# Performance work log

Hardware: AMD Instinct MI355X
Metric: run time of the kernel (lower is better)

The kernel has to match this reference:

```python
import math
import jax, jax.numpy as jnp
import numpy as np

HIDDEN = 1024
HEADS = 16
HEAD = HIDDEN // HEADS
BUCKET = 32
MAXPOS = 512
REL = 2 * BUCKET - 1
EPS = 1e-7
L, B = 512, 16
STD = math.sqrt(2.0 / (5.0 * HIDDEN))


def _ln(x, g=None, b=None):
    m = x.mean(-1, keepdims=True)
    v = ((x - m) ** 2).mean(-1, keepdims=True)
    y = (x - m) * jax.lax.rsqrt(v + EPS)
    return y if g is None else y * g + b


def _bucket_indices(n):
    # DeBERTa-style log bucket relative positions, shifted to [0, 2*BUCKET-2]
    r = jnp.arange(n)[:, None] - jnp.arange(n)[None, :]
    mid = BUCKET // 2
    abs_pos = jnp.where((r < mid) & (r > -mid), mid - 1,
                        jnp.clip(jnp.abs(r), None, MAXPOS - 1))
    log_pos = jnp.ceil(jnp.log(abs_pos.astype(jnp.float32) / mid)
                       / math.log((MAXPOS - 1) / mid) * (mid - 1)).astype(jnp.int32) + mid
    bucket_pos = jnp.where(abs_pos <= mid, r, log_pos * jnp.sign(r))
    return (BUCKET - 1 + bucket_pos).astype(jnp.int32)


def setup_inputs() -> dict:
    key = jax.random.key(0)
    ks = jax.random.split(key, 8)
    return {
        'hidden_states': jax.random.normal(ks[0], (L, B, HIDDEN), jnp.float32),
        'attention_mask': jax.random.randint(ks[1], (B, 1, 1, L), 0, 2).astype(bool),
        'relative_embedding': jax.random.normal(ks[2], (REL, HIDDEN), jnp.float32),
        'wqk': jax.random.normal(ks[3], (2 * HIDDEN, HIDDEN), jnp.float32) * STD,
        'bqk': jnp.zeros((2 * HIDDEN,), jnp.float32),
        'wv': jax.random.normal(ks[4], (HIDDEN, HIDDEN), jnp.float32) * STD,
        'bv': jnp.zeros((HIDDEN,), jnp.float32),
        'wo': jax.random.normal(ks[5], (HIDDEN, HIDDEN), jnp.float32) * STD,
        'bo': jnp.zeros((HIDDEN,), jnp.float32),
        'ln_g': jnp.ones((HIDDEN,), jnp.float32),
        'ln_b': jnp.zeros((HIDDEN,), jnp.float32),
    }


def reference(hidden_states, attention_mask, relative_embedding,
              wqk, bqk, wv, bv, wo, bo, ln_g, ln_b):
    Lq, Bq, D = hidden_states.shape
    scale = 1.0 / math.sqrt(3 * HEAD)
    h = _ln(hidden_states)                                 # pre LN, no affine
    q, k = jnp.split(h @ wqk.T + bqk, 2, axis=-1)
    v = h @ wv.T + bv
    qpos, kpos = jnp.split(relative_embedding @ wqk.T + bqk, 2, axis=-1)
    qpos = qpos.reshape(REL, HEADS, HEAD)
    kpos = kpos.reshape(REL, HEADS, HEAD)
    # (L,B,D) -> (B,H,L,hd)
    qh = q.reshape(Lq, Bq, HEADS, HEAD).transpose(1, 2, 0, 3)
    kh = k.reshape(Lq, Bq, HEADS, HEAD).transpose(1, 2, 0, 3)
    vh = v.reshape(Lq, Bq, HEADS, HEAD).transpose(1, 2, 0, 3)
    scores = jnp.einsum('bhqd,bhkd->bhqk', qh, kh) * scale       # c2c
    qp = jnp.einsum('bhqd,khd->bhqk', qh, kpos) * scale          # c2p (k over buckets)
    pk = jnp.einsum('bhkd,qhd->bhqk', kh, qpos) * scale          # p2c (q over buckets)
    idx = jnp.broadcast_to(_bucket_indices(Lq), (Bq, HEADS, Lq, Lq))
    scores = scores + jnp.take_along_axis(qp, idx, axis=-1) \
                    + jnp.take_along_axis(pk, idx, axis=-2)
    # masked softmax: mask==True -> -inf before softmax, 0 after
    probs = jax.nn.softmax(jnp.where(attention_mask, -1e9, scores), axis=-1)
    probs = jnp.where(attention_mask, 0.0, probs)
    ctx = jnp.einsum('bhqk,bhkd->bhqd', probs, vh)
    ctx = ctx.transpose(2, 0, 1, 3).reshape(Lq, Bq, D)           # (L,B,D)
    out = ctx @ wo.T + bo
    return _ln(out, ln_g, ln_b)
```

## Files before the change

### kernel.cpp

```cpp
#include <hip/hip_runtime.h>
#include <hip/hip_bf16.h>

#define HID 1024
#define HEADS 16
#define HEAD 64
#define RELN 63
#define SEQ 512
#define BATCH 16
#define NROWS (SEQ*BATCH)
#define MEXT 8320
#define NQKV 3072
#define LNEPS 1e-7f
#define SCALE2 (0.07216878364870323f * 1.4426950408889634f)

typedef __attribute__((ext_vector_type(4))) float  f32x4;
typedef __attribute__((ext_vector_type(8))) short  s16x8;
typedef __attribute__((ext_vector_type(4))) ushort u16x4;

static __device__ __forceinline__ ushort f2bf(float f) {
  union { float f; unsigned u; } v; v.f = f;
  unsigned r = v.u + 0x7fffu + ((v.u >> 16) & 1u);
  return (ushort)(r >> 16);
}
static __device__ __forceinline__ float bf2f(ushort u) {
  union { unsigned u; float f; } v; v.u = ((unsigned)u) << 16;
  return v.f;
}

__global__ void k_prep(const void* mask_raw, const float* bqk, const float* bv,
                       ushort* mask01, int* idx_tab, float* bcat) {
  __shared__ int s_isbool;
  int tid = threadIdx.x;
  if (tid == 0) s_isbool = 0;
  __syncthreads();
  const unsigned* mu = (const unsigned*)mask_raw;
  int bad = 0;
  for (int i = tid; i < 2048; i += 256) if (mu[i] > 1u) bad = 1;
  if (bad) s_isbool = 1;
  __syncthreads();
  int isbool = s_isbool;
  const unsigned char* m8 = (const unsigned char*)mask_raw;
  const int* m32 = (const int*)mask_raw;
  for (int i = tid; i < BATCH*SEQ; i += 256) {
    int m = isbool ? (int)m8[i] : m32[i];
    mask01[i] = m ? 1 : 0;
  }
  for (int i = tid; i < 1023; i += 256) {
    int r = i - 511;
    int a = r < 0 ? -r : r;
    int absp = (a < 16) ? 15 : (a < 511 ? a : 511);
    int idx;
    if (absp <= 16) idx = 31 + r;
    else {
      float v = logf((float)absp / 16.0f) / logf(511.0f / 16.0f) * 15.0f;
      int lp = (int)ceilf(v) + 16;
      idx = 31 + (r > 0 ? lp : -lp);
    }
    idx_tab[i] = idx;
  }
  for (int i = tid; i < 2048; i += 256) bcat[i] = bqk[i];
  for (int i = tid; i < 1024; i += 256) bcat[2048 + i] = bv[i];
}

__global__ __launch_bounds__(256) void k_convert(const float* wqk, const float* wv, const float* wo,
                                                 ushort* wcat, ushort* wo_b) {
  int c = blockIdx.x * 256 + threadIdx.x;
  f32x4 x; ushort* dst;
  if (c < 524288)      { x = *(const f32x4*)(wqk + (size_t)c * 4);            dst = wcat + (size_t)c * 4; }
  else if (c < 786432) { x = *(const f32x4*)(wv  + (size_t)(c - 524288) * 4); dst = wcat + (size_t)c * 4; }
  else                 { x = *(const f32x4*)(wo  + (size_t)(c - 786432) * 4); dst = wo_b + (size_t)(c - 786432) * 4; }
  u16x4 o = { f2bf(x[0]), f2bf(x[1]), f2bf(x[2]), f2bf(x[3]) };
  *(u16x4*)dst = o;
}

__global__ __launch_bounds__(256) void k_ln1(const float* hid, const float* rel, ushort* h_ext) {
  int row = blockIdx.x, tid = threadIdx.x;
  __shared__ float red[8];
  if (row < NROWS) {
    const float* src = hid + (size_t)row * HID;
    f32x4 x = *(const f32x4*)(src + tid * 4);
    float s = x[0] + x[1] + x[2] + x[3];
    #pragma unroll
    for (int m = 1; m < 64; m <<= 1) s += __shfl_xor(s, m);
    if ((tid & 63) == 0) red[tid >> 6] = s;
    __syncthreads();
    float mean = (red[0] + red[1] + red[2] + red[3]) * (1.0f / HID);
    float d0 = x[0] - mean, d1 = x[1] - mean, d2 = x[2] - mean, d3 = x[3] - mean;
    float sq = d0*d0 + d1*d1 + d2*d2 + d3*d3;
    #pragma unroll
    for (int m = 1; m < 64; m <<= 1) sq += __shfl_xor(sq, m);
    __syncthreads();
    if ((tid & 63) == 0) red[4 + (tid >> 6)] = sq;
    __syncthreads();
    float var = (red[4] + red[5] + red[6] + red[7]) * (1.0f / HID);
    float rs = rsqrtf(var + LNEPS);
    u16x4 o = { f2bf(d0*rs), f2bf(d1*rs), f2bf(d2*rs), f2bf(d3*rs) };
    *(u16x4*)(h_ext + (size_t)row * HID + tid * 4) = o;
  } else if (row < NROWS + RELN) {
    const float* src = rel + (size_t)(row - NROWS) * HID;
    f32x4 x = *(const f32x4*)(src + tid * 4);
    u16x4 o = { f2bf(x[0]), f2bf(x[1]), f2bf(x[2]), f2bf(x[3]) };
    *(u16x4*)(h_ext + (size_t)row * HID + tid * 4) = o;
  } else {
    u16x4 z = { 0, 0, 0, 0 };
    *(u16x4*)(h_ext + (size_t)row * HID + tid * 4) = z;
  }
}

template<int WRITE_F32>
__global__ __launch_bounds__(256) void k_gemm(const ushort* A, const ushort* Bw, const float* bias,
                                              ushort* Cb, float* Cf, int M, int N, int K) {
  __shared__ char smem[32768];
  char* As = smem;
  char* Bs = smem + 16384;
  int tid = threadIdx.x, lane = tid & 63, w = tid >> 6;
  int nbn = N >> 7;
  int per = gridDim.x >> 3;
  int gl = (blockIdx.x & 7) * per + (blockIdx.x >> 3);
  int bm = gl / nbn, bn = gl % nbn;
  int wr = w >> 1, wc = w & 1;
  int g = lane >> 4, r = lane & 15;
  f32x4 acc[4][4] = {};
  for (int ko = 0; ko < K; ko += 64) {
    __syncthreads();
    #pragma unroll
    for (int c = 0; c < 4; ++c) {
      int chunk = c * 256 + tid;
      int row = chunk >> 3;
      int kb = (chunk & 7) << 4;
      int kbs = kb ^ ((row & 7) << 4);
      const char* gA = (const char*)(A + (size_t)(bm * 128 + row) * K + ko) + kbs;
      const char* gB = (const char*)(Bw + (size_t)(bn * 128 + row) * K + ko) + kbs;
      __builtin_amdgcn_global_load_lds((const __attribute__((address_space(1))) void*)gA,
                                       (__attribute__((address_space(3))) void*)(As + c * 4096 + w * 1024),
                                       16, 0, 0);
      __builtin_amdgcn_global_load_lds((const __attribute__((address_space(1))) void*)gB,
                                       (__attribute__((address_space(3))) void*)(Bs + c * 4096 + w * 1024),
                                       16, 0, 0);
    }
    __syncthreads();
    #pragma unroll
    for (int kk = 0; kk < 2; ++kk) {
      s16x8 af[4], bf[4];
      #pragma unroll
      for (int mt = 0; mt < 4; ++mt) {
        int row = wr * 64 + mt * 16 + r;
        int kb = (kk * 64 + g * 16) ^ ((row & 7) << 4);
        af[mt] = *(const s16x8*)(As + row * 128 + kb);
      }
      #pragma unroll
      for (int nt = 0; nt < 4; ++nt) {
        int row = wc * 64 + nt * 16 + r;
        int kb = (kk * 64 + g * 16) ^ ((row & 7) << 4);
        bf[nt] = *(const s16x8*)(Bs + row * 128 + kb);
      }
      #pragma unroll
      for (int mt = 0; mt < 4; ++mt)
        #pragma unroll
        for (int nt = 0; nt < 4; ++nt)
          acc[mt][nt] = __builtin_amdgcn_mfma_f32_16x16x32_bf16(af[mt], bf[nt], acc[mt][nt], 0, 0, 0);
    }
  }
  #pragma unroll
  for (int nt = 0; nt < 4; ++nt) {
    int col = bn * 128 + wc * 64 + nt * 16 + r;
    float bvv = bias[col];
    #pragma unroll
    for (int mt = 0; mt < 4; ++mt) {
      int row0 = bm * 128 + wr * 64 + mt * 16 + g * 4;
      #pragma unroll
      for (int i = 0; i < 4; ++i) {
        float v = acc[mt][nt][i] + bvv;
        if (WRITE_F32) Cf[(size_t)(row0 + i) * N + col] = v;
        else           Cb[(size_t)(row0 + i) * N + col] = f2bf(v);
      }
    }
  }
}

__global__ __launch_bounds__(256) void k_pos(const ushort* qkv, const ushort* mask01,
                                             ushort* qp, ushort* pk) {
  int bh = blockIdx.x;
  int b = bh >> 4, h = bh & 15;
  int tid = threadIdx.x, lane = tid & 63, w = tid >> 6;
  int g = lane >> 4, r = lane & 15;
  __shared__ ushort mb[512];
  for (int i = tid; i < 512; i += 256) mb[i] = mask01[b * SEQ + i];
  __syncthreads();
  s16x8 bkp[4][2], bqp[4][2];
  #pragma unroll
  for (int nt = 0; nt < 4; ++nt)
    #pragma unroll
    for (int kk = 0; kk < 2; ++kk) {
      size_t rowp = (size_t)(NROWS + nt * 16 + r);
      int colq = h * 64 + kk * 32 + g * 8;
      bqp[nt][kk] = *(const s16x8*)(qkv + rowp * NQKV + colq);
      bkp[nt][kk] = *(const s16x8*)(qkv + rowp * NQKV + 1024 + colq);
    }
  for (int cc = 0; cc < 8; ++cc) {
    int rowbase = cc * 64 + w * 16;
    s16x8 aq[2], ak[2];
    #pragma unroll
    for (int kk = 0; kk < 2; ++kk) {
      size_t rowq = (size_t)((rowbase + r) * 16 + b);
      int colq = h * 64 + kk * 32 + g * 8;
      aq[kk] = *(const s16x8*)(qkv + rowq * NQKV + colq);
      ak[kk] = *(const s16x8*)(qkv + rowq * NQKV + 1024 + colq);
    }
    f32x4 accq[4] = {}, acck[4] = {};
    #pragma unroll
    for (int kk = 0; kk < 2; ++kk)
      #pragma unroll
      for (int nt = 0; nt < 4; ++nt) {
        accq[nt] = __builtin_amdgcn_mfma_f32_16x16x32_bf16(aq[kk], bkp[nt][kk], accq[nt], 0, 0, 0);
        acck[nt] = __builtin_amdgcn_mfma_f32_16x16x32_bf16(ak[kk], bqp[nt][kk], acck[nt], 0, 0, 0);
      }
    #pragma unroll
    for (int nt = 0; nt < 4; ++nt)
      #pragma unroll
      for (int i = 0; i < 4; ++i) {
        int q = rowbase + g * 4 + i;
        int t = nt * 16 + r;
        float biasv = mb[q] ? -1e9f : 0.0f;
        qp[(size_t)bh * SEQ * 64 + q * 64 + t] = f2bf(accq[nt][i] * SCALE2);
        pk[(size_t)bh * SEQ * 64 + q * 64 + t] = f2bf(acck[nt][i] * SCALE2 + biasv);
      }
  }
}

__global__ __launch_bounds__(256) void k_vt(const ushort* qkv, ushort* vt, ushort* kc) {
  int bid = blockIdx.x;
  int bh = bid >> 3, lt = bid & 7;
  int b = bh >> 4, h = bh & 15;
  __shared__ ushort tile[64][72];
  int tid = threadIdx.x;
  #pragma unroll
  for (int c = 0; c < 2; ++c) {
    int e = (c * 256 + tid) * 8;
    int l = e >> 6, d0 = e & 63;
    size_t row = (size_t)((lt * 64 + l) * 16 + b);
    s16x8 kv = *(const s16x8*)(qkv + row * NQKV + 1024 + h * 64 + d0);
    #pragma unroll
    for (int j = 0; j < 8; ++j) kv[j] = (short)f2bf(bf2f((ushort)kv[j]) * SCALE2);
    *(s16x8*)(kc + ((size_t)bh * SEQ + lt * 64 + l) * 64 + d0) = kv;
    *(s16x8*)&tile[l][d0] = *(const s16x8*)(qkv + row * NQKV + 2048 + h * 64 + d0);
  }
  __syncthreads();
  #pragma unroll
  for (int c = 0; c < 2; ++c) {
    int e = (c * 256 + tid) * 8;
    int d = e >> 6, l0 = e & 63;
    ushort tmp[8];
    #pragma unroll
    for (int j = 0; j < 8; ++j) tmp[j] = tile[l0 + j][d];
    *(s16x8*)(vt + (size_t)(bh * 64 + d) * SEQ + lt * 64 + l0) = *(s16x8*)tmp;
  }
}

__global__ __launch_bounds__(512) void k_attn(const ushort* qkv, const ushort* qp_all, const ushort* pk_all,
                                              const ushort* kc, const ushort* vt,
                                              const int* idx_tab, ushort* ctx) {
  int bid = blockIdx.x;
  int slot = bid >> 3;
  int bh = (bid & 7) * 32 + (slot >> 1);
  int qh = slot & 1;
  int b = bh >> 4, h = bh & 15;
  int tid = threadIdx.x, lane = tid & 63, w = tid >> 6;
  int g = lane >> 4, r = lane & 15;

  __shared__ ushort pk_f[512][68];
  __shared__ ushort qp_s[256][68];
  __shared__ ushort p_s[8][16][68];
  __shared__ ushort idx_s[1024];

  const ushort* qpsrc = qp_all + (size_t)bh * SEQ * 64 + (size_t)qh * 256 * 64;
  const ushort* pksrc = pk_all + (size_t)bh * SEQ * 64;
  const char*   kcb   = (const char*)(kc + (size_t)bh * SEQ * 64);

  #pragma unroll
  for (int c = 0; c < 4; ++c) {
    int chunk = c * 512 + tid;
    int row = chunk >> 3, col8 = (chunk & 7) * 8;
    s16x8 v = *(const s16x8*)(qpsrc + (size_t)row * 64 + col8);
    u16x4 lo = { (ushort)v[0], (ushort)v[1], (ushort)v[2], (ushort)v[3] };
    u16x4 hi = { (ushort)v[4], (ushort)v[5], (ushort)v[6], (ushort)v[7] };
    *(u16x4*)&qp_s[row][col8] = lo;
    *(u16x4*)&qp_s[row][col8 + 4] = hi;
  }
  #pragma unroll
  for (int c = 0; c < 8; ++c) {
    int chunk = c * 512 + tid;
    int row = chunk >> 3, col8 = (chunk & 7) * 8;
    s16x8 v = *(const s16x8*)(pksrc + (size_t)row * 64 + col8);
    u16x4 lo = { (ushort)v[0], (ushort)v[1], (ushort)v[2], (ushort)v[3] };
    u16x4 hi = { (ushort)v[4], (ushort)v[5], (ushort)v[6], (ushort)v[7] };
    *(u16x4*)&pk_f[row][col8] = lo;
    *(u16x4*)&pk_f[row][col8 + 4] = hi;
  }
  for (int i = tid; i < 1023; i += 512) idx_s[i] = (ushort)idx_tab[i];
  s16x8 aq[2][2];
  #pragma unroll
  for (int qs = 0; qs < 2; ++qs)
    #pragma unroll
    for (int kk = 0; kk < 2; ++kk) {
      int qglob = qh * 256 + qs * 128 + w * 16 + r;
      aq[qs][kk] = *(const s16x8*)(qkv + ((size_t)qglob * 16 + b) * NQKV + h * 64 + kk * 32 + g * 8);
    }
  __syncthreads();

  float m_i[2] = { -3e38f, -3e38f }, l_i[2] = { 0.0f, 0.0f };
  f32x4 o_acc[2][4] = {};

  for (int kt = 0; kt < 8; ++kt) {
    s16x8 kf[4][2], vf[2][4];
    #pragma unroll
    for (int nt = 0; nt < 4; ++nt)
      #pragma unroll
      for (int kk = 0; kk < 2; ++kk)
        kf[nt][kk] = *(const s16x8*)(kcb + (size_t)(kt * 64 + nt * 16 + r) * 128 + kk * 64 + g * 16);
    #pragma unroll
    for (int kk = 0; kk < 2; ++kk)
      #pragma unroll
      for (int nt = 0; nt < 4; ++nt)
        vf[kk][nt] = *(const s16x8*)(vt + (size_t)(bh * 64 + nt * 16 + r) * SEQ + kt * 64 + kk * 32 + g * 8);

    #pragma unroll
    for (int qs = 0; qs < 2; ++qs) {
      f32x4 s[4];
      #pragma unroll
      for (int nt = 0; nt < 4; ++nt) {
        f32x4 a = {};
        #pragma unroll
        for (int kk = 0; kk < 2; ++kk)
          a = __builtin_amdgcn_mfma_f32_16x16x32_bf16(kf[nt][kk], aq[qs][kk], a, 0, 0, 0);
        s[nt] = a;
      }

      const ushort* qprow = &qp_s[qs * 128 + w * 16 + r][0];
      const int qg511 = qh * 256 + qs * 128 + w * 16 + r + 511;
      float m_loc = -3e38f;
      #pragma unroll
      for (int nt = 0; nt < 4; ++nt) {
        #pragma unroll
        for (int i = 0; i < 4; ++i) {
          int kg = kt * 64 + nt * 16 + g * 4 + i;
          int t = idx_s[qg511 - kg];
          float v = s[nt][i] + bf2f(qprow[t]) + bf2f(pk_f[kg][t]);
          s[nt][i] = v;
          m_loc = fmaxf(m_loc, v);
        }
      }

      float mx = fmaxf(m_loc, __shfl_xor(m_loc, 16));
      mx = fmaxf(mx, __shfl_xor(mx, 32));

      if (__any(mx > m_i[qs] + 8.0f)) {
        float mnew = fmaxf(m_i[qs], mx);
        float rs = exp2f(m_i[qs] - mnew);
        m_i[qs] = mnew;
        l_i[qs] *= rs;
        float rsb[4];
        #pragma unroll
        for (int i = 0; i < 4; ++i) rsb[i] = __shfl(rs, g * 4 + i);
        #pragma unroll
        for (int nt = 0; nt < 4; ++nt)
          #pragma unroll
          for (int i = 0; i < 4; ++i) o_acc[qs][nt][i] *= rsb[i];
      }

      float psum = 0.0f;
      #pragma unroll
      for (int nt = 0; nt < 4; ++nt) {
        u16x4 pk4;
        #pragma unroll
        for (int i = 0; i < 4; ++i) {
          float pe = exp2f(s[nt][i] - m_i[qs]);
          psum += pe;
          pk4[i] = f2bf(pe);
        }
        *(u16x4*)&p_s[w][r][nt * 16 + g * 4] = pk4;
      }
      psum += __shfl_xor(psum, 16);
      psum += __shfl_xor(psum, 32);
      l_i[qs] += psum;

      #pragma unroll
      for (int kk = 0; kk < 2; ++kk) {
        u16x4 lo = *(const u16x4*)&p_s[w][r][kk * 32 + g * 8];
        u16x4 hi = *(const u16x4*)&p_s[w][r][kk * 32 + g * 8 + 4];
        s16x8 pa = { (short)lo[0], (short)lo[1], (short)lo[2], (short)lo[3],
                     (short)hi[0], (short)hi[1], (short)hi[2], (short)hi[3] };
        #pragma unroll
        for (int nt = 0; nt < 4; ++nt)
          o_acc[qs][nt] = __builtin_amdgcn_mfma_f32_16x16x32_bf16(pa, vf[kk][nt], o_acc[qs][nt], 0, 0, 0);
      }
    }
  }

  #pragma unroll
  for (int qs = 0; qs < 2; ++qs) {
    float lb[4];
    #pragma unroll
    for (int i = 0; i < 4; ++i) lb[i] = __shfl(l_i[qs], g * 4 + i);
    #pragma unroll
    for (int i = 0; i < 4; ++i) {
      float inv = lb[i] > 0.0f ? 1.0f / lb[i] : 0.0f;
      int lq = qh * 256 + qs * 128 + w * 16 + g * 4 + i;
      size_t rowc = (size_t)(lq * 16 + b);
      #pragma unroll
      for (int nt = 0; nt < 4; ++nt)
        ctx[rowc * HID + h * 64 + nt * 16 + r] = f2bf(o_acc[qs][nt][i] * inv);
    }
  }
}

__global__ __launch_bounds__(256) void k_ln2(const ushort* tmpb, const float* gamma, const float* beta,
                                             float* out) {
  int row = blockIdx.x, tid = threadIdx.x;
  __shared__ float red[8];
  u16x4 xb = *(const u16x4*)(tmpb + (size_t)row * HID + tid * 4);
  float x[4] = { bf2f(xb[0]), bf2f(xb[1]), bf2f(xb[2]), bf2f(xb[3]) };
  float s = x[0] + x[1] + x[2] + x[3];
  #pragma unroll
  for (int m = 1; m < 64; m <<= 1) s += __shfl_xor(s, m);
  if ((tid & 63) == 0) red[tid >> 6] = s;
  __syncthreads();
  float mean = (red[0] + red[1] + red[2] + red[3]) * (1.0f / HID);
  float d[4]; float sq = 0.0f;
  #pragma unroll
  for (int j = 0; j < 4; ++j) { d[j] = x[j] - mean; sq += d[j] * d[j]; }
  #pragma unroll
  for (int m = 1; m < 64; m <<= 1) sq += __shfl_xor(sq, m);
  __syncthreads();
  if ((tid & 63) == 0) red[4 + (tid >> 6)] = sq;
  __syncthreads();
  float var = (red[4] + red[5] + red[6] + red[7]) * (1.0f / HID);
  float rs = rsqrtf(var + LNEPS);
  f32x4 o;
  #pragma unroll
  for (int j = 0; j < 4; ++j) o[j] = d[j] * rs * gamma[tid * 4 + j] + beta[tid * 4 + j];
  *(f32x4*)(out + (size_t)row * HID + tid * 4) = o;
}

extern "C" void kernel_launch(void* const* d_in, const int* in_sizes, int n_in,
                              void* d_out, int out_size, void* d_ws, size_t ws_size,
                              hipStream_t stream) {
  (void)in_sizes; (void)n_in; (void)out_size; (void)ws_size;
  const float* hid  = (const float*)d_in[0];
  const void*  mask = d_in[1];
  const float* rel  = (const float*)d_in[2];
  const float* wqk  = (const float*)d_in[3];
  const float* bqk  = (const float*)d_in[4];
  const float* wv   = (const float*)d_in[5];
  const float* bv   = (const float*)d_in[6];
  const float* wo   = (const float*)d_in[7];
  const float* bo   = (const float*)d_in[8];
  const float* ln_g = (const float*)d_in[9];
  const float* ln_b = (const float*)d_in[10];

  char* ws = (char*)d_ws;
  ushort* wcat     = (ushort*)(ws);
  ushort* wo_b     = (ushort*)(ws + 6291456);
  float*  bcat     = (float*) (ws + 8388608);
  ushort* mask01   = (ushort*)(ws + 8400896);
  int*    idx_tab  = (int*)   (ws + 8433664);
  ushort* h_ext    = (ushort*)(ws + 8437760);
  ushort* qkv      = (ushort*)(ws + 25477120);
  ushort* qp_b     = (ushort*)(ws + 76595200);
  ushort* pk_b     = (ushort*)(ws + 93372416);
  ushort* vt       = (ushort*)(ws + 110149632);
  char*   tmpr     = (ws + 126926848);
  ushort* ctx = h_ext;
  ushort* kc   = (ushort*)tmpr;
  ushort* tmpb = (ushort*)tmpr;

  k_prep<<<1, 256, 0, stream>>>(mask, bqk, bv, mask01, idx_tab, bcat);
  k_convert<<<4096, 256, 0, stream>>>(wqk, wv, wo, wcat, wo_b);
  k_ln1<<<MEXT, 256, 0, stream>>>(hid, rel, h_ext);
  k_gemm<0><<<(MEXT / 128) * (NQKV / 128), 256, 0, stream>>>(h_ext, wcat, bcat, qkv, nullptr, MEXT, NQKV, 1024);
  k_pos<<<256, 256, 0, stream>>>(qkv, mask01, qp_b, pk_b);
  k_vt<<<2048, 256, 0, stream>>>(qkv, vt, kc);
  k_attn<<<512, 512, 0, stream>>>(qkv, qp_b, pk_b, kc, vt, idx_tab, ctx);
  k_gemm<0><<<(NROWS / 128) * (1024 / 128), 256, 0, stream>>>(ctx, wo_b, bo, tmpb, nullptr, NROWS, 1024, 1024);
  k_ln2<<<NROWS, 256, 0, stream>>>(tmpb, ln_g, ln_b, (float*)d_out);
}
```

Measured before the change: 255.6 us.

## Use 256x128 tiles for QKV GEMM and split-K for output projection

```diff
diff --git a/kernel.cpp b/kernel.cpp
--- a/kernel.cpp
+++ b/kernel.cpp
@@ -107,12 +107,11 @@
   }
 }
 
-template<int WRITE_F32>
-__global__ __launch_bounds__(256) void k_gemm(const ushort* A, const ushort* Bw, const float* bias,
-                                              ushort* Cb, float* Cf, int M, int N, int K) {
-  __shared__ char smem[32768];
+__global__ __launch_bounds__(512) void k_gemm256(const ushort* A, const ushort* Bw, const float* bias,
+                                                 ushort* Cb, int M, int N, int K) {
+  __shared__ char smem[49152];
   char* As = smem;
-  char* Bs = smem + 16384;
+  char* Bs = smem + 32768;
   int tid = threadIdx.x, lane = tid & 63, w = tid >> 6;
   int nbn = N >> 7;
   int per = gridDim.x >> 3;
@@ -125,10 +124,84 @@
     __syncthreads();
     #pragma unroll
     for (int c = 0; c < 4; ++c) {
+      int chunk = c * 512 + tid;
+      int row = chunk >> 3;
+      int kbs = ((chunk & 7) << 4) ^ ((row & 7) << 4);
+      int ar = bm * 256 + row; ar = ar < M ? ar : M - 1;
+      const char* gA = (const char*)(A + (size_t)ar * K + ko) + kbs;
+      __builtin_amdgcn_global_load_lds((const __attribute__((address_space(1))) void*)gA,
+                                       (__attribute__((address_space(3))) void*)(As + c * 8192 + w * 1024),
+                                       16, 0, 0);
+    }
+    #pragma unroll
+    for (int c = 0; c < 2; ++c) {
+      int chunk = c * 512 + tid;
+      int row = chunk >> 3;
+      int kbs = ((chunk & 7) << 4) ^ ((row & 7) << 4);
+      const char* gB = (const char*)(Bw + (size_t)(bn * 128 + row) * K + ko) + kbs;
+      __builtin_amdgcn_global_load_lds((const __attribute__((address_space(1))) void*)gB,
+                                       (__attribute__((address_space(3))) void*)(Bs + c * 8192 + w * 1024),
+                                       16, 0, 0);
+    }
+    __syncthreads();
+    #pragma unroll
+    for (int kk = 0; kk < 2; ++kk) {
+      s16x8 af[4], bf[4];
+      #pragma unroll
+      for (int mt = 0; mt < 4; ++mt) {
+        int row = wr * 64 + mt * 16 + r;
+        int kb = (kk * 64 + g * 16) ^ ((row & 7) << 4);
+        af[mt] = *(const s16x8*)(As + row * 128 + kb);
+      }
+      #pragma unroll
+      for (int nt = 0; nt < 4; ++nt) {
+        int row = wc * 64 + nt * 16 + r;
+        int kb = (kk * 64 + g * 16) ^ ((row & 7) << 4);
+        bf[nt] = *(const s16x8*)(Bs + row * 128 + kb);
+      }
+      #pragma unroll
+      for (int mt = 0; mt < 4; ++mt)
+        #pragma unroll
+        for (int nt = 0; nt < 4; ++nt)
+          acc[mt][nt] = __builtin_amdgcn_mfma_f32_16x16x32_bf16(af[mt], bf[nt], acc[mt][nt], 0, 0, 0);
+    }
+  }
+  #pragma unroll
+  for (int nt = 0; nt < 4; ++nt) {
+    int col = bn * 128 + wc * 64 + nt * 16 + r;
+    float bvv = bias[col];
+    #pragma unroll
+    for (int mt = 0; mt < 4; ++mt) {
+      int row0 = bm * 256 + wr * 64 + mt * 16 + g * 4;
+      #pragma unroll
+      for (int i = 0; i < 4; ++i) {
+        int row = row0 + i;
+        if (row < M) Cb[(size_t)row * N + col] = f2bf(acc[mt][nt][i] + bvv);
+      }
+    }
+  }
+}
+
+__global__ __launch_bounds__(256) void k_gemm_sk(const ushort* A, const ushort* Bw, const float* bias,
+                                                 ushort* C0, ushort* C1) {
+  const int N = 1024, K = 1024;
+  __shared__ char smem[32768];
+  char* As = smem;
+  char* Bs = smem + 16384;
+  int tid = threadIdx.x, lane = tid & 63, w = tid >> 6;
+  int per = gridDim.x >> 3;
+  int gl = (blockIdx.x & 7) * per + (blockIdx.x >> 3);
+  int bn = gl & 7, ks = (gl >> 3) & 1, bm = gl >> 4;
+  int wr = w >> 1, wc = w & 1;
+  int g = lane >> 4, r = lane & 15;
+  f32x4 acc[4][4] = {};
+  for (int ko = ks * 512; ko < ks * 512 + 512; ko += 64) {
+    __syncthreads();
+    #pragma unroll
+    for (int c = 0; c < 4; ++c) {
       int chunk = c * 256 + tid;
       int row = chunk >> 3;
-      int kb = (chunk & 7) << 4;
-      int kbs = kb ^ ((row & 7) << 4);
+      int kbs = ((chunk & 7) << 4) ^ ((row & 7) << 4);
       const char* gA = (const char*)(A + (size_t)(bm * 128 + row) * K + ko) + kbs;
       const char* gB = (const char*)(Bw + (size_t)(bn * 128 + row) * K + ko) + kbs;
       __builtin_amdgcn_global_load_lds((const __attribute__((address_space(1))) void*)gA,
@@ -161,19 +234,17 @@
           acc[mt][nt] = __builtin_amdgcn_mfma_f32_16x16x32_bf16(af[mt], bf[nt], acc[mt][nt], 0, 0, 0);
     }
   }
+  ushort* C = ks ? C1 : C0;
   #pragma unroll
   for (int nt = 0; nt < 4; ++nt) {
     int col = bn * 128 + wc * 64 + nt * 16 + r;
-    float bvv = bias[col];
+    float bvv = ks ? 0.0f : bias[col];
     #pragma unroll
     for (int mt = 0; mt < 4; ++mt) {
       int row0 = bm * 128 + wr * 64 + mt * 16 + g * 4;
       #pragma unroll
-      for (int i = 0; i < 4; ++i) {
-        float v = acc[mt][nt][i] + bvv;
-        if (WRITE_F32) Cf[(size_t)(row0 + i) * N + col] = v;
-        else           Cb[(size_t)(row0 + i) * N + col] = f2bf(v);
-      }
+      for (int i = 0; i < 4; ++i)
+        C[(size_t)(row0 + i) * N + col] = f2bf(acc[mt][nt][i] + bvv);
     }
   }
 }
@@ -414,12 +485,15 @@
   }
 }
 
-__global__ __launch_bounds__(256) void k_ln2(const ushort* tmpb, const float* gamma, const float* beta,
-                                             float* out) {
+__global__ __launch_bounds__(256) void k_ln2(const ushort* t0, const ushort* t1,
+                                             const float* gamma, const float* beta, float* out) {
   int row = blockIdx.x, tid = threadIdx.x;
   __shared__ float red[8];
-  u16x4 xb = *(const u16x4*)(tmpb + (size_t)row * HID + tid * 4);
-  float x[4] = { bf2f(xb[0]), bf2f(xb[1]), bf2f(xb[2]), bf2f(xb[3]) };
+  u16x4 xa = *(const u16x4*)(t0 + (size_t)row * HID + tid * 4);
+  u16x4 xb = *(const u16x4*)(t1 + (size_t)row * HID + tid * 4);
+  float x[4];
+  #pragma unroll
+  for (int j = 0; j < 4; ++j) x[j] = bf2f(xa[j]) + bf2f(xb[j]);
   float s = x[0] + x[1] + x[2] + x[3];
   #pragma unroll
   for (int m = 1; m < 64; m <<= 1) s += __shfl_xor(s, m);
@@ -472,15 +546,16 @@
   char*   tmpr     = (ws + 126926848);
   ushort* ctx = h_ext;
   ushort* kc   = (ushort*)tmpr;
-  ushort* tmpb = (ushort*)tmpr;
+  ushort* tmp0 = (ushort*)tmpr;
+  ushort* tmp1 = (ushort*)(tmpr + 16777216);
 
   k_prep<<<1, 256, 0, stream>>>(mask, bqk, bv, mask01, idx_tab, bcat);
   k_convert<<<4096, 256, 0, stream>>>(wqk, wv, wo, wcat, wo_b);
   k_ln1<<<MEXT, 256, 0, stream>>>(hid, rel, h_ext);
-  k_gemm<0><<<(MEXT / 128) * (NQKV / 128), 256, 0, stream>>>(h_ext, wcat, bcat, qkv, nullptr, MEXT, NQKV, 1024);
+  k_gemm256<<<33 * (NQKV / 128), 512, 0, stream>>>(h_ext, wcat, bcat, qkv, MEXT, NQKV, 1024);
   k_pos<<<256, 256, 0, stream>>>(qkv, mask01, qp_b, pk_b);
   k_vt<<<2048, 256, 0, stream>>>(qkv, vt, kc);
   k_attn<<<512, 512, 0, stream>>>(qkv, qp_b, pk_b, kc, vt, idx_tab, ctx);
-  k_gemm<0><<<(NROWS / 128) * (1024 / 128), 256, 0, stream>>>(ctx, wo_b, bo, tmpb, nullptr, NROWS, 1024, 1024);
-  k_ln2<<<NROWS, 256, 0, stream>>>(tmpb, ln_g, ln_b, (float*)d_out);
-}
+  k_gemm_sk<<<1024, 256, 0, stream>>>(ctx, wo_b, bo, tmp0, tmp1);
+  k_ln2<<<NROWS, 256, 0, stream>>>(tmp0, tmp1, ln_g, ln_b, (float*)d_out);
+}
```

Result: no change. 255.1 us (-0.2%).
